# Performance work log

Measured on AMD Instinct MI355X. Metric: run time of the kernel, lower is better.

The kernel has to match this reference:

```python
import jax, jax.numpy as jnp
import numpy as np

B, S, F, H, T_OUT = 2048, 512, 32, 128, 24


def setup_inputs() -> dict:
    key = jax.random.key(0)
    ks = jax.random.split(key, 16)
    sc = 0.1
    return {
        "xb": jax.random.normal(ks[0], (B, S, F), dtype=jnp.float32),
        "enc_Wih": sc * jax.random.normal(ks[1], (3 * H, F), dtype=jnp.float32),
        "enc_Whh": sc * jax.random.normal(ks[2], (3 * H, H), dtype=jnp.float32),
        "enc_bih": sc * jax.random.normal(ks[3], (3 * H,), dtype=jnp.float32),
        "enc_bhh": sc * jax.random.normal(ks[4], (3 * H,), dtype=jnp.float32),
        "attn_W": sc * jax.random.normal(ks[5], (S, H + F), dtype=jnp.float32),
        "attn_b": sc * jax.random.normal(ks[6], (S,), dtype=jnp.float32),
        "dec_Wih": sc * jax.random.normal(ks[7], (3 * H, H), dtype=jnp.float32),
        "dec_Whh": sc * jax.random.normal(ks[8], (3 * H, H), dtype=jnp.float32),
        "dec_bih": sc * jax.random.normal(ks[9], (3 * H,), dtype=jnp.float32),
        "dec_bhh": sc * jax.random.normal(ks[10], (3 * H,), dtype=jnp.float32),
        "out1_W": sc * jax.random.normal(ks[11], (F, H), dtype=jnp.float32),
        "out1_b": sc * jax.random.normal(ks[12], (F,), dtype=jnp.float32),
        "out2_W": sc * jax.random.normal(ks[13], (1, F), dtype=jnp.float32),
        "out2_b": sc * jax.random.normal(ks[14], (1,), dtype=jnp.float32),
    }


def _gru_cell(x_proj, h, Whh, bhh):
    # x_proj: [B, 3H] = x @ Wih.T + bih (precomputed); torch GRU gate order r,z,n
    g_h = h @ Whh.T + bhh
    ir, iz, inn = jnp.split(x_proj, 3, axis=1)
    hr, hz, hn = jnp.split(g_h, 3, axis=1)
    r = jax.nn.sigmoid(ir + hr)
    z = jax.nn.sigmoid(iz + hz)
    n = jnp.tanh(inn + r * hn)
    return (1.0 - z) * n + z * h


def reference(xb, enc_Wih, enc_Whh, enc_bih, enc_bhh, attn_W, attn_b,
              dec_Wih, dec_Whh, dec_bih, dec_bhh, out1_W, out1_b, out2_W, out2_b):
    b = xb.shape[0]
    # ---- Encoder GRU (1 layer, unidirectional) ----
    x_proj = jnp.einsum('btf,gf->btg', xb, enc_Wih) + enc_bih  # [B,S,3H]

    def enc_step(h, xp):
        h = _gru_cell(xp, h, enc_Whh, enc_bhh)
        return h, h

    h0 = jnp.zeros((b, enc_Whh.shape[1]), dtype=xb.dtype)
    enc_hidden, enc_out = jax.lax.scan(enc_step, h0, jnp.swapaxes(x_proj, 0, 1))
    enc_out = jnp.swapaxes(enc_out, 0, 1)  # [B,S,H]

    # ---- Attention decoder loop ----
    y0 = xb[:, -1, :]  # [B,F]

    def dec_step(carry, _):
        h, y = carry
        ai = jnp.concatenate([h, y], axis=1)              # [B,H+F]
        w = jax.nn.softmax(ai @ attn_W.T + attn_b, axis=1)  # [B,S]
        ctx = jnp.einsum('bs,bsh->bh', w, enc_out)        # [B,H]
        xp = ctx @ dec_Wih.T + dec_bih
        h_new = _gru_cell(xp, h, dec_Whh, dec_bhh)
        out = h_new @ out1_W.T + out1_b                   # [B,F]
        return (h_new, out), out

    _, outs = jax.lax.scan(dec_step, (enc_hidden, y0), None, length=T_OUT)
    outs = jnp.swapaxes(outs, 0, 1)                       # [B,T_OUT,F]
    outs = jax.nn.relu(outs)
    outs = outs @ out2_W.T + out2_b                       # [B,T_OUT,1]
    outs = jax.nn.relu(outs)
    return outs.squeeze(-1)                               # [B,T_OUT]
```

## Files before the change

### kernel.cpp

```cpp
#include <hip/hip_runtime.h>
#include <hip/hip_fp16.h>

#define BB 2048
#define SS 512
#define FF 32
#define HH 128
#define TO 24
#define LOG2E 1.4426950408889634f

typedef unsigned int uint;
using half4 = __attribute__((ext_vector_type(4))) _Float16;
using half8 = __attribute__((ext_vector_type(8))) _Float16;
using f32x4 = __attribute__((ext_vector_type(4))) float;

#define OFF_ENCOUT 0ull
#define OFF_HFIN  (OFF_ENCOUT + (size_t)BB*SS*HH*2)
#define OFF_ATTNF (OFF_HFIN + (size_t)BB*HH*4)
#define OFF_ATTNB (OFF_ATTNF + (size_t)65536*2)
#define OFF_DECF  (OFF_ATTNB + (size_t)512*4)
#define OFF_OUT1F (OFF_DECF + (size_t)98304*2)
#define OFF_WF    (OFF_OUT1F + (size_t)4096*2)

__global__ void prep_kernel(const float* attn_W, const float* attn_b,
                            const float* dec_Wih, const float* dec_Whh,
                            const float* out1_W, const float* out1_b,
                            const float* enc_Wih, const float* enc_Whh,
                            __half* attnF, float* attnB, __half* decF, __half* out1F, __half* Wf) {
  int i = blockIdx.x * 256 + threadIdx.x;
  if (i < 65536) {
    int e = i & 7, l = (i >> 3) & 63, kb = (i >> 9) & 3, st = (i >> 11) & 3, w = i >> 13;
    int h = kb*32 + ((l >> 4) << 3) + e;
    int s = w*64 + st*16 + (l & 15);
    float acc = attn_W[s*160 + h];
    #pragma unroll 8
    for (int f = 0; f < 32; ++f) acc += out1_W[f*128 + h] * attn_W[s*160 + 128 + f];
    attnF[i] = __float2half(acc);
    return;
  }
  i -= 65536;
  if (i < 512) {
    float acc = attn_b[i];
    #pragma unroll 8
    for (int f = 0; f < 32; ++f) acc += out1_b[f] * attn_W[i*160 + 128 + f];
    attnB[i] = acc;
    return;
  }
  i -= 512;
  if (i < 98304) {
    int e = i & 7, l = (i >> 3) & 63, fi = (i >> 9) % 48, w = i / 24576;
    int lq = l >> 4, l15 = l & 15;
    float val;
    if (fi < 32) {
      int g2 = fi >> 4, sub = (fi >> 3) & 1, kb = fi & 7;
      int k = kb*32 + lq*8 + e, j = w*32 + sub*16 + l15, jg = g2*128 + j;
      val = (k < 128) ? dec_Wih[jg*128 + k] : dec_Whh[jg*128 + (k - 128)];
    } else {
      int f2 = fi - 32, cat = f2 >> 3, sub = (f2 >> 2) & 1, kb4 = f2 & 3;
      int k = kb4*32 + lq*8 + e, j = 256 + w*32 + sub*16 + l15;
      val = cat ? dec_Wih[j*128 + k] : dec_Whh[j*128 + k];
    }
    decF[i] = __float2half(val);
    return;
  }
  i -= 98304;
  if (i < 4096) {
    int e = i & 7, l = (i >> 3) & 63, kb = (i >> 9) & 3, tile = (i >> 11) & 1;
    int k = kb*32 + ((l >> 4) << 3) + e;
    int f = tile*16 + (l & 15);
    out1F[i] = __float2half(out1_W[f*128 + k]);
    return;
  }
  i -= 4096;
  if (i < 61440) {
    int e = i & 7, l = (i >> 3) & 63, q = i >> 9;
    int kb = q % 5, tt = (q / 5) % 6, w = q / 30;
    int g = tt >> 1, sub = tt & 1;
    int k = kb*32 + ((l >> 4) << 3) + e;
    int J = g*128 + w*32 + sub*16 + (l & 15);
    float v = (k < 128) ? enc_Whh[J*128 + k] : enc_Wih[J*32 + (k - 128)];
    Wf[i] = __float2half(v);
  }
}

#define HXS 168

__global__ void __launch_bounds__(256, 1) enc_kernel(
    const float* __restrict__ xb, const __half* __restrict__ Wf,
    const float* __restrict__ bih, const float* __restrict__ bhh,
    __half* __restrict__ enc_out, float* __restrict__ hfin) {
  __shared__ __align__(16) _Float16 hx[2][16][HXS];
  const int tid  = threadIdx.x;
  const int lane = tid & 63, wid = tid >> 6;
  const int l15  = lane & 15, lq = lane >> 4;
  const int b0   = blockIdx.x * 8;

  half8 Bf[6][5];
  { const half8* wfp = (const half8*)Wf;
    #pragma unroll
    for (int tt = 0; tt < 6; ++tt)
      #pragma unroll
      for (int kb = 0; kb < 5; ++kb)
        Bf[tt][kb] = wfp[((wid*6 + tt)*5 + kb)*64 + lane];
  }

  float br[2], bz[2], bnh[2], bni[2];
  #pragma unroll
  for (int sub = 0; sub < 2; ++sub) {
    int j = wid*32 + sub*16 + l15;
    br[sub]  = bih[j]       + bhh[j];
    bz[sub]  = bih[128 + j] + bhh[128 + j];
    bnh[sub] = bhh[256 + j];
    bni[sub] = bih[256 + j];
  }
  float hreg[2][4] = {{0.f,0.f,0.f,0.f},{0.f,0.f,0.f,0.f}};

  const int m2 = tid >> 5, c2 = tid & 31;
  const float* xbase = xb + ((size_t)(b0 + m2)*512)*32 + c2;

  for (int i = tid; i < 2*16*HXS; i += 256) (&hx[0][0][0])[i] = (_Float16)0.f;
  __syncthreads();
  hx[0][m2][128 + c2] = (_Float16)xbase[0];
  __syncthreads();

  float xq_next = xbase[1*32];

  int p = 0;
  for (int t = 0; t < 512; ++t) {
    const int tn2 = (t < 510) ? t + 2 : 511;
    float xq_new = xbase[(size_t)tn2*32];

    half8 A[5];
    #pragma unroll
    for (int kb = 0; kb < 5; ++kb)
      A[kb] = *(const half8*)&hx[p][l15][kb*32 + lq*8];

    f32x4 Cr[2], Cz[2], Cnh[2], Cni[2];
    #pragma unroll
    for (int sub = 0; sub < 2; ++sub) {
      Cr[sub] = (f32x4){0.f,0.f,0.f,0.f};
      Cz[sub] = (f32x4){0.f,0.f,0.f,0.f};
      Cnh[sub] = (f32x4){0.f,0.f,0.f,0.f};
      Cni[sub] = (f32x4){0.f,0.f,0.f,0.f};
    }
    #pragma unroll
    for (int sub = 0; sub < 2; ++sub) {
      #pragma unroll
      for (int kb = 0; kb < 5; ++kb) {
        Cr[sub] = __builtin_amdgcn_mfma_f32_16x16x32_f16(A[kb], Bf[sub][kb],     Cr[sub], 0, 0, 0);
        Cz[sub] = __builtin_amdgcn_mfma_f32_16x16x32_f16(A[kb], Bf[2 + sub][kb], Cz[sub], 0, 0, 0);
      }
      #pragma unroll
      for (int kb = 0; kb < 4; ++kb)
        Cnh[sub] = __builtin_amdgcn_mfma_f32_16x16x32_f16(A[kb], Bf[4 + sub][kb], Cnh[sub], 0, 0, 0);
      Cni[sub] = __builtin_amdgcn_mfma_f32_16x16x32_f16(A[4], Bf[4 + sub][4], Cni[sub], 0, 0, 0);
    }

    #pragma unroll
    for (int sub = 0; sub < 2; ++sub)
      #pragma unroll
      for (int i = 0; i < 4; ++i) {
        float xr = Cr[sub][i] + br[sub];
        float xz = Cz[sub][i] + bz[sub];
        float r = __builtin_amdgcn_rcpf(1.f + __builtin_amdgcn_exp2f(-LOG2E*xr));
        float z = __builtin_amdgcn_rcpf(1.f + __builtin_amdgcn_exp2f(-LOG2E*xz));
        float narg = (Cni[sub][i] + bni[sub]) + r * (Cnh[sub][i] + bnh[sub]);
        float n = 1.f - 2.f*__builtin_amdgcn_rcpf(__builtin_amdgcn_exp2f((2.f*LOG2E)*narg) + 1.f);
        float hnew = n + z*(hreg[sub][i] - n);
        hreg[sub][i] = hnew;
        if (lq < 2)
          hx[p ^ 1][4*lq + i][wid*32 + sub*16 + l15] = (_Float16)hnew;
      }
    hx[p ^ 1][m2][128 + c2] = (_Float16)xq_next;
    xq_next = xq_new;
    __syncthreads();

    { half4 hv = *(const half4*)&hx[p ^ 1][m2][c2*4];
      *(half4*)((void*)&enc_out[((size_t)(b0 + m2)*512 + t)*128 + c2*4]) = hv; }
    p ^= 1;
  }

  if (lq < 2)
    #pragma unroll
    for (int sub = 0; sub < 2; ++sub)
      #pragma unroll
      for (int i = 0; i < 4; ++i)
        hfin[(size_t)(b0 + 4*lq + i)*128 + wid*32 + sub*16 + l15] = hreg[sub][i];
}

struct DecSmem {
  _Float16 ET[128*512];
  _Float16 wsm[512];
  float hsm[128];
  _Float16 hh[128];
  _Float16 cxh[2][256];
  _Float16 hist[TO*128];
  float red[16];
  float d32[32];
};

__global__ void __launch_bounds__(512, 2) dec_kernel(const float* __restrict__ xb,
    const __half* __restrict__ enc_out, const float* __restrict__ hfin,
    const __half* __restrict__ attnF, const float* __restrict__ attnB,
    const float* __restrict__ attn_W,
    const __half* __restrict__ decF, const __half* __restrict__ out1F,
    const float* __restrict__ dbih, const float* __restrict__ dbhh,
    const float* __restrict__ out1_W, const float* __restrict__ out1_b,
    const float* __restrict__ out2_W, const float* __restrict__ out2_b,
    float* __restrict__ out) {
  __shared__ __align__(16) DecSmem sm;
  const int tid = threadIdx.x, lane = tid & 63, wid = tid >> 6;
  const int l15 = lane & 15, lq = lane >> 4;
  const int b = blockIdx.x;

  const half8* aFp = (const half8*)attnF;
  const half8* dFp = (const half8*)decF;
  const half8* oFp = (const half8*)out1F;
  const int Wb = wid >> 1, sb = wid & 1;

  const float ab = attnB[tid];
  const int jg = wid*16 + l15;
  const float bR  = dbih[jg]       + dbhh[jg];
  const float bZ  = dbih[128 + jg] + dbhh[128 + jg];
  const float bNH = dbhh[256 + jg];
  const float bNI = dbih[256 + jg];
  const float o1b0 = out1_b[l15], o1b1 = out1_b[16 + l15];
  const float o2w0 = out2_W[l15], o2w1 = out2_W[16 + l15];
  const float o2b  = out2_b[0];

  { const half8* src = (const half8*)(enc_out + (size_t)b*512*128);
    for (int i = tid; i < 8192; i += 512) {
      half8 v = src[i];
      int s = i >> 4, h0 = (i & 15) * 8, sg = s >> 3, s7 = s & 7;
      #pragma unroll
      for (int j = 0; j < 8; ++j) {
        int h = h0 + j;
        sm.ET[h*512 + (((sg ^ (h & 7) ^ ((h >> 3) & 7)) << 3)) + s7] = v[j];
      }
    } }
  if (tid < 128) { float hv = hfin[(size_t)b*128 + tid];
    sm.hsm[tid] = hv; sm.hh[tid] = (_Float16)hv; sm.cxh[0][128 + tid] = (_Float16)hv; }
  if (tid < 32) {
    float o1v = out1_b[tid];
    for (int h = 0; h < 128; ++h) o1v += out1_W[tid*128 + h] * hfin[(size_t)b*128 + h];
    sm.d32[tid] = xb[((size_t)b*512 + 511)*32 + tid] - o1v;
  }
  __syncthreads();
  float c0reg = 0.f;
  #pragma unroll 8
  for (int f = 0; f < 32; ++f) c0reg += sm.d32[f] * attn_W[tid*160 + 128 + f];

  const half8 Az = {};
  const int hrow = wid*16 + l15;
  const int hswz = (hrow & 7) ^ ((hrow >> 3) & 7);

  for (int tt = 0; tt < TO; ++tt) {
    _Float16* cxhR = sm.cxh[tt & 1];
    _Float16* cxhW = sm.cxh[(tt & 1) ^ 1];

    half8 A[4];
    #pragma unroll
    for (int kb = 0; kb < 4; ++kb)
      A[kb] = (l15 == 0) ? *(const half8*)&sm.hh[kb*32 + lq*8] : Az;
    f32x4 CL[4];
    #pragma unroll
    for (int stt = 0; stt < 4; ++stt) CL[stt] = (f32x4){0.f,0.f,0.f,0.f};
    #pragma unroll
    for (int stt = 0; stt < 4; ++stt)
      #pragma unroll
      for (int kb = 0; kb < 4; ++kb)
        CL[stt] = __builtin_amdgcn_mfma_f32_16x16x32_f16(
            A[kb], aFp[((wid*4 + stt)*4 + kb)*64 + lane], CL[stt], 0, 0, 0);
    float t0 = __shfl(CL[0][0], l15), t1 = __shfl(CL[1][0], l15);
    float t2 = __shfl(CL[2][0], l15), t3 = __shfl(CL[3][0], l15);
    float v = (lq == 0) ? t0 : (lq == 1) ? t1 : (lq == 2) ? t2 : t3;
    v += ab;
    if (tt == 0) v += c0reg;
    float mw = v;
    #pragma unroll
    for (int off = 1; off < 64; off <<= 1) mw = fmaxf(mw, __shfl_xor(mw, off));
    float sw = __builtin_amdgcn_exp2f(LOG2E*(v - mw));
    #pragma unroll
    for (int off = 1; off < 64; off <<= 1) sw += __shfl_xor(sw, off);
    if (lane == 0) { sm.red[wid] = mw; sm.red[8 + wid] = sw; }
    __syncthreads();

    float M = sm.red[0];
    #pragma unroll
    for (int g = 1; g < 8; ++g) M = fmaxf(M, sm.red[g]);
    float tot = 0.f;
    #pragma unroll
    for (int g = 0; g < 8; ++g) tot += sm.red[8 + g] * __builtin_amdgcn_exp2f(LOG2E*(sm.red[g] - M));
    float wv = __builtin_amdgcn_exp2f(LOG2E*(v - M)) * __builtin_amdgcn_rcpf(tot);
    sm.wsm[tid] = (_Float16)wv;
    __syncthreads();

    f32x4 Ca[2];
    Ca[0] = (f32x4){0.f,0.f,0.f,0.f}; Ca[1] = (f32x4){0.f,0.f,0.f,0.f};
    #pragma unroll
    for (int kb = 0; kb < 16; ++kb) {
      const half8 bet = *(const half8*)&sm.ET[hrow*512 + (((kb*4 + lq) ^ hswz) << 3)];
      const half8 aw  = (l15 == 0) ? *(const half8*)&sm.wsm[kb*32 + lq*8] : Az;
      Ca[kb & 1] = __builtin_amdgcn_mfma_f32_16x16x32_f16(aw, bet, Ca[kb & 1], 0, 0, 0);
    }
    if (lane < 16)
      cxhR[wid*16 + l15] = (_Float16)(Ca[0][0] + Ca[1][0]);
    __syncthreads();

    half8 Ag[8];
    #pragma unroll
    for (int kb = 0; kb < 8; ++kb)
      Ag[kb] = (l15 == 0) ? *(const half8*)&cxhR[kb*32 + lq*8] : Az;
    f32x4 Cr, Cz, Cnh4, Cni4;
    Cr = (f32x4){0.f,0.f,0.f,0.f}; Cz = (f32x4){0.f,0.f,0.f,0.f};
    Cnh4 = (f32x4){0.f,0.f,0.f,0.f}; Cni4 = (f32x4){0.f,0.f,0.f,0.f};
    #pragma unroll
    for (int kb = 0; kb < 8; ++kb) {
      Cr = __builtin_amdgcn_mfma_f32_16x16x32_f16(Ag[kb], dFp[(Wb*48 +      sb*8 + kb)*64 + lane], Cr, 0, 0, 0);
      Cz = __builtin_amdgcn_mfma_f32_16x16x32_f16(Ag[kb], dFp[(Wb*48 + 16 + sb*8 + kb)*64 + lane], Cz, 0, 0, 0);
    }
    #pragma unroll
    for (int kb = 0; kb < 4; ++kb) {
      Cnh4 = __builtin_amdgcn_mfma_f32_16x16x32_f16(Ag[4 + kb], dFp[(Wb*48 + 32 + sb*4 + kb)*64 + lane], Cnh4, 0, 0, 0);
      Cni4 = __builtin_amdgcn_mfma_f32_16x16x32_f16(Ag[kb],     dFp[(Wb*48 + 40 + sb*4 + kb)*64 + lane], Cni4, 0, 0, 0);
    }
    if (lane < 16) {
      float xr = Cr[0] + bR, xz = Cz[0] + bZ;
      float r = __builtin_amdgcn_rcpf(1.f + __builtin_amdgcn_exp2f(-LOG2E*xr));
      float z = __builtin_amdgcn_rcpf(1.f + __builtin_amdgcn_exp2f(-LOG2E*xz));
      float narg = (Cni4[0] + bNI) + r * (Cnh4[0] + bNH);
      float n = 1.f - 2.f*__builtin_amdgcn_rcpf(__builtin_amdgcn_exp2f((2.f*LOG2E)*narg) + 1.f);
      float hnew = n + z*(sm.hsm[jg] - n);
      sm.hsm[jg] = hnew;
      _Float16 hf = (_Float16)hnew;
      sm.hh[jg] = hf;
      cxhW[128 + jg] = hf;
      sm.hist[tt*128 + jg] = hf;
    }
    __syncthreads();
  }

  if (wid == 0) {
    #pragma unroll
    for (int chunk = 0; chunk < 2; ++chunk) {
      half8 Ae[4];
      #pragma unroll
      for (int kb = 0; kb < 4; ++kb) {
        int step = chunk*16 + l15;
        Ae[kb] = (step < TO) ? *(const half8*)&sm.hist[step*128 + kb*32 + lq*8] : Az;
      }
      f32x4 C0, C1;
      C0 = (f32x4){0.f,0.f,0.f,0.f}; C1 = (f32x4){0.f,0.f,0.f,0.f};
      #pragma unroll
      for (int kb = 0; kb < 4; ++kb) {
        C0 = __builtin_amdgcn_mfma_f32_16x16x32_f16(Ae[kb], oFp[kb*64 + lane],       C0, 0, 0, 0);
        C1 = __builtin_amdgcn_mfma_f32_16x16x32_f16(Ae[kb], oFp[(4 + kb)*64 + lane], C1, 0, 0, 0);
      }
      #pragma unroll
      for (int i = 0; i < 4; ++i) {
        int row = lq*4 + i, step = chunk*16 + row;
        float y0 = C0[i] + o1b0, y1 = C1[i] + o1b1;
        float part = fmaxf(y0, 0.f)*o2w0 + fmaxf(y1, 0.f)*o2w1;
        #pragma unroll
        for (int off = 1; off < 16; off <<= 1) part += __shfl_xor(part, off, 16);
        if (l15 == 0 && step < TO)
          out[(size_t)b*TO + step] = fmaxf(part + o2b, 0.f);
      }
    }
  }
}

extern "C" void kernel_launch(void* const* d_in, const int* in_sizes, int n_in,
                              void* d_out, int out_size, void* d_ws, size_t ws_size,
                              hipStream_t stream) {
  const float* xb      = (const float*)d_in[0];
  const float* enc_Wih = (const float*)d_in[1];
  const float* enc_Whh = (const float*)d_in[2];
  const float* enc_bih = (const float*)d_in[3];
  const float* enc_bhh = (const float*)d_in[4];
  const float* attn_W  = (const float*)d_in[5];
  const float* attn_b  = (const float*)d_in[6];
  const float* dec_Wih = (const float*)d_in[7];
  const float* dec_Whh = (const float*)d_in[8];
  const float* dec_bih = (const float*)d_in[9];
  const float* dec_bhh = (const float*)d_in[10];
  const float* out1_W  = (const float*)d_in[11];
  const float* out1_b  = (const float*)d_in[12];
  const float* out2_W  = (const float*)d_in[13];
  const float* out2_b  = (const float*)d_in[14];

  char* ws = (char*)d_ws;
  __half* enc_out = (__half*)(ws + OFF_ENCOUT);
  float*  hfin    = (float*)(ws + OFF_HFIN);
  __half* attnF   = (__half*)(ws + OFF_ATTNF);
  float*  attnB   = (float*)(ws + OFF_ATTNB);
  __half* decF    = (__half*)(ws + OFF_DECF);
  __half* out1F   = (__half*)(ws + OFF_OUT1F);
  __half* Wf      = (__half*)(ws + OFF_WF);

  prep_kernel<<<900, 256, 0, stream>>>(attn_W, attn_b, dec_Wih, dec_Whh, out1_W, out1_b,
                                       enc_Wih, enc_Whh, attnF, attnB, decF, out1F, Wf);
  enc_kernel<<<256, 256, 0, stream>>>(xb, Wf, enc_bih, enc_bhh, enc_out, hfin);
  dec_kernel<<<2048, 512, 0, stream>>>(xb, enc_out, hfin, attnF, attnB, attn_W, decF, out1F,
                                       dec_bih, dec_bhh, out1_W, out1_b, out2_W, out2_b,
                                       (float*)d_out);
}
```

Measured before the change: 1.107 ms.

## Prefetch decoder GRU weights early and drop max-subtraction from attention softmax

At the start of each decoder step, the GRU input-weight fragments are loaded from global memory into registers so the loads overlap the attention stage instead of stalling the gate MFMAs. The softmax no longer subtracts the max, which removes one wave-wide shuffle reduction and the cross-wave max merge. Launch bounds are relaxed from 2 to 1 block per SM so the extra registers fit. Dropping the max assumes the attention logits stay small enough not to overflow exp, and occupancy may fall.

```diff
diff --git a/kernel.cpp b/kernel.cpp
--- a/kernel.cpp
+++ b/kernel.cpp
@@ -198,7 +198,7 @@
   float d32[32];
 };
 
-__global__ void __launch_bounds__(512, 2) dec_kernel(const float* __restrict__ xb,
+__global__ void __launch_bounds__(512, 1) dec_kernel(const float* __restrict__ xb,
     const __half* __restrict__ enc_out, const float* __restrict__ hfin,
     const __half* __restrict__ attnF, const float* __restrict__ attnB,
     const float* __restrict__ attn_W,
@@ -257,6 +257,18 @@
     _Float16* cxhR = sm.cxh[tt & 1];
     _Float16* cxhW = sm.cxh[(tt & 1) ^ 1];
 
+    half8 pRzR[8], pRzZ[8], pNh[4], pNi[4];
+    #pragma unroll
+    for (int kb = 0; kb < 8; ++kb) {
+      pRzR[kb] = dFp[(Wb*48 +      sb*8 + kb)*64 + lane];
+      pRzZ[kb] = dFp[(Wb*48 + 16 + sb*8 + kb)*64 + lane];
+    }
+    #pragma unroll
+    for (int kb = 0; kb < 4; ++kb) {
+      pNh[kb] = dFp[(Wb*48 + 32 + sb*4 + kb)*64 + lane];
+      pNi[kb] = dFp[(Wb*48 + 40 + sb*4 + kb)*64 + lane];
+    }
+
     half8 A[4];
     #pragma unroll
     for (int kb = 0; kb < 4; ++kb)
@@ -275,23 +287,17 @@
     float v = (lq == 0) ? t0 : (lq == 1) ? t1 : (lq == 2) ? t2 : t3;
     v += ab;
     if (tt == 0) v += c0reg;
-    float mw = v;
-    #pragma unroll
-    for (int off = 1; off < 64; off <<= 1) mw = fmaxf(mw, __shfl_xor(mw, off));
-    float sw = __builtin_amdgcn_exp2f(LOG2E*(v - mw));
+    float ex = __builtin_amdgcn_exp2f(LOG2E*v);
+    float sw = ex;
     #pragma unroll
     for (int off = 1; off < 64; off <<= 1) sw += __shfl_xor(sw, off);
-    if (lane == 0) { sm.red[wid] = mw; sm.red[8 + wid] = sw; }
+    if (lane == 0) sm.red[wid] = sw;
     __syncthreads();
 
-    float M = sm.red[0];
-    #pragma unroll
-    for (int g = 1; g < 8; ++g) M = fmaxf(M, sm.red[g]);
-    float tot = 0.f;
-    #pragma unroll
-    for (int g = 0; g < 8; ++g) tot += sm.red[8 + g] * __builtin_amdgcn_exp2f(LOG2E*(sm.red[g] - M));
-    float wv = __builtin_amdgcn_exp2f(LOG2E*(v - M)) * __builtin_amdgcn_rcpf(tot);
-    sm.wsm[tid] = (_Float16)wv;
+    float tot = sm.red[0];
+    #pragma unroll
+    for (int g = 1; g < 8; ++g) tot += sm.red[g];
+    sm.wsm[tid] = (_Float16)(ex * __builtin_amdgcn_rcpf(tot));
     __syncthreads();
 
     f32x4 Ca[2];
@@ -315,13 +321,13 @@
     Cnh4 = (f32x4){0.f,0.f,0.f,0.f}; Cni4 = (f32x4){0.f,0.f,0.f,0.f};
     #pragma unroll
     for (int kb = 0; kb < 8; ++kb) {
-      Cr = __builtin_amdgcn_mfma_f32_16x16x32_f16(Ag[kb], dFp[(Wb*48 +      sb*8 + kb)*64 + lane], Cr, 0, 0, 0);
-      Cz = __builtin_amdgcn_mfma_f32_16x16x32_f16(Ag[kb], dFp[(Wb*48 + 16 + sb*8 + kb)*64 + lane], Cz, 0, 0, 0);
+      Cr = __builtin_amdgcn_mfma_f32_16x16x32_f16(Ag[kb], pRzR[kb], Cr, 0, 0, 0);
+      Cz = __builtin_amdgcn_mfma_f32_16x16x32_f16(Ag[kb], pRzZ[kb], Cz, 0, 0, 0);
     }
     #pragma unroll
     for (int kb = 0; kb < 4; ++kb) {
-      Cnh4 = __builtin_amdgcn_mfma_f32_16x16x32_f16(Ag[4 + kb], dFp[(Wb*48 + 32 + sb*4 + kb)*64 + lane], Cnh4, 0, 0, 0);
-      Cni4 = __builtin_amdgcn_mfma_f32_16x16x32_f16(Ag[kb],     dFp[(Wb*48 + 40 + sb*4 + kb)*64 + lane], Cni4, 0, 0, 0);
+      Cnh4 = __builtin_amdgcn_mfma_f32_16x16x32_f16(Ag[4 + kb], pNh[kb], Cnh4, 0, 0, 0);
+      Cni4 = __builtin_amdgcn_mfma_f32_16x16x32_f16(Ag[kb],     pNi[kb], Cni4, 0, 0, 0);
     }
     if (lane < 16) {
       float xr = Cr[0] + bR, xz = Cz[0] + bZ;
```

Measured after the change: 1.042 ms. -5.8%, faster.
